# Optimization experiments

Hardware: AMD Instinct MI355X
Metric: run time of the kernel (lower is better)

## Reference

```python
import jax, jax.numpy as jnp
import numpy as np

A_CONST = 0.4
C_CONST = 500.0
N_BINS = 10


def entropy(w):
    # Faithful to the torch helper: n=10 half-open bins [min+i*s, min+(i+1)*s);
    # the maximum element falls outside the last bin, as in the original.
    x = w.reshape(-1)
    lo = x.min()
    hi = x.max()
    scale = (hi - lo) / N_BINS
    i = jnp.arange(N_BINS, dtype=x.dtype)
    lower = lo + i * scale            # [n]
    upper = lo + (i + 1.0) * scale    # [n]
    in_bin = (x[None, :] >= lower[:, None]) & (x[None, :] < upper[:, None])  # [n, len]
    p = jnp.sum(in_bin, axis=1).astype(jnp.float32) / x.shape[0]
    return jnp.sum(jnp.where(p > 0, -p * jnp.log(p), 0.0))


def blend_weight(base_w, graft_w, pnet_w):
    # param_direction = |base - graft| passed through bias-free Linear(in, in)
    d = jnp.abs(base_w - graft_w) @ pnet_w.T          # [out, in]
    w_local = jax.nn.sigmoid(d)
    w_global = A_CONST / jnp.pi * jnp.arctan(C_CONST * (entropy(base_w) - entropy(graft_w))) + 0.5
    w_base = w_global * (1.0 - jnp.exp(-w_global * w_local))
    w_graft = (1.0 - w_global) * (1.0 - jnp.exp(-(1.0 - w_global) * (1.0 - w_local)))
    ws = jax.nn.softmax(jnp.stack([w_base, w_graft], axis=-1), axis=-1)  # [out, in, 2]
    return base_w * ws[..., 0] + graft_w * ws[..., 1]


def setup_inputs() -> dict:
    key = jax.random.key(0)
    ks = jax.random.split(key, 9)
    B, D_IN, D_H, D_OUT = 65536, 1024, 512, 1
    return {
        "x": jax.random.normal(ks[0], (B, D_IN), dtype=jnp.float32),
        "w0": jax.random.normal(ks[1], (D_H, D_IN), dtype=jnp.float32) * 0.05,
        "b0": jax.random.normal(ks[2], (D_H,), dtype=jnp.float32) * 0.05,
        "w1": jax.random.normal(ks[3], (D_OUT, D_H), dtype=jnp.float32) * 0.05,
        "b1": jax.random.normal(ks[4], (D_OUT,), dtype=jnp.float32) * 0.05,
        "p0": jax.random.normal(ks[5], (D_IN, D_IN), dtype=jnp.float32) * 0.05,
        "p1": jax.random.normal(ks[6], (D_H, D_H), dtype=jnp.float32) * 0.05,
        "g0": jax.random.normal(ks[7], (D_H, D_IN), dtype=jnp.float32) * 0.05,
        "g1": jax.random.normal(ks[8], (D_OUT, D_H), dtype=jnp.float32) * 0.05,
    }


def reference(x, w0, b0, w1, b1, p0, p1, g0, g1):
    W0 = blend_weight(w0, g0, p0)
    x = jax.nn.relu(x @ W0.T + b0)   # layer 0 + ReLU
    W1 = blend_weight(w1, g1, p1)
    x = x @ W1.T + b1                # layer 1, no activation
    return x
```

## Files before the change

kernel.cpp:

```cpp
#include <hip/hip_runtime.h>
#include <hip/hip_bf16.h>
#include <math.h>


typedef __attribute__((ext_vector_type(8))) short short8;
typedef __attribute__((ext_vector_type(4))) short short4v;
typedef __attribute__((ext_vector_type(4))) float floatx4;
typedef unsigned short ushort_t;

#define WS_CNT 16
#define WS_PART 64
#define WS_PART2 576
#define WS_W0T 1024
#define WS_W1B (WS_W0T + 262144)

__device__ __forceinline__ short f2bf(float f) {
    union { __hip_bfloat16 h; short s; } u;
    u.h = __float2bfloat16(f);
    return u.s;
}
__device__ __forceinline__ float blend_factor(float d, float wg) {
    float wl = 1.0f / (1.0f + expf(-d));
    float wb = wg * (1.0f - expf(-wg * wl));
    float wgr = (1.0f - wg) * (1.0f - expf(-(1.0f - wg) * (1.0f - wl)));
    return 1.0f / (1.0f + expf(-(wb - wgr)));
}
__device__ __forceinline__ float wglobal_from_ent(float eb, float eg) {
    return 0.12732395447351627f * atanf(500.0f * (eb - eg)) + 0.5f;
}
__device__ __forceinline__ void async16(const void* g, void* s) {
    __builtin_amdgcn_global_load_lds(
        (const __attribute__((address_space(1))) unsigned int*)g,
        (__attribute__((address_space(3))) unsigned int*)s, 16, 0, 0);
}
__device__ __forceinline__ int swz_idx(int h, int k) {
    int kq = (k >> 3) & 3;
    return h * 32 + (((kq ^ ((h >> 1) & 3))) << 3) + (k & 7);
}

__global__ __launch_bounds__(256) void k_mm(const float* __restrict__ w0,
                                            const float* __restrict__ g0,
                                            const float* __restrict__ w1,
                                            const float* __restrict__ g1,
                                            unsigned* ws_u) {
    float* ws_f = (float*)ws_u;
    __shared__ float smn[4], smx[4];
    int bx = blockIdx.x, tid = threadIdx.x;
    int wave = tid >> 6, lane = tid & 63;
    int a = bx >> 7;
    const float* arr = (a ? g0 : w0) + (size_t)(bx & 127) * 4096;
    float mn = INFINITY, mx = -INFINITY;
    const float4* p4 = (const float4*)arr;
#pragma unroll
    for (int j = 0; j < 4; j++) {
        float4 v = p4[tid + j * 256];
        mn = fminf(mn, fminf(fminf(v.x, v.y), fminf(v.z, v.w)));
        mx = fmaxf(mx, fmaxf(fmaxf(v.x, v.y), fmaxf(v.z, v.w)));
    }
#pragma unroll
    for (int off = 32; off > 0; off >>= 1) {
        mn = fminf(mn, __shfl_xor(mn, off));
        mx = fmaxf(mx, __shfl_xor(mx, off));
    }
    if (lane == 0) { smn[wave] = mn; smx[wave] = mx; }
    __syncthreads();
    if (tid == 0) {
        mn = fminf(fminf(smn[0], smn[1]), fminf(smn[2], smn[3]));
        mx = fmaxf(fmaxf(smx[0], smx[1]), fmaxf(smx[2], smx[3]));
        ws_f[WS_PART + bx * 2] = mn;
        ws_f[WS_PART + bx * 2 + 1] = mx;
    }
    if (bx < 2 && tid < 64) {
        const float* arr2 = bx ? g1 : w1;
        float mn2 = INFINITY, mx2 = -INFINITY;
#pragma unroll
        for (int j = 0; j < 8; j++) {
            float v = arr2[tid + 64 * j];
            mn2 = fminf(mn2, v);
            mx2 = fmaxf(mx2, v);
        }
#pragma unroll
        for (int off = 32; off > 0; off >>= 1) {
            mn2 = fminf(mn2, __shfl_xor(mn2, off));
            mx2 = fmaxf(mx2, __shfl_xor(mx2, off));
        }
        if (tid == 0) {
            ws_f[WS_PART2 + bx * 2] = mn2;
            ws_f[WS_PART2 + bx * 2 + 1] = mx2;
        }
    }
    if (bx == 2 && tid < 40) ws_u[WS_CNT + tid] = 0u;
}

__global__ __launch_bounds__(256) void k_hist(const float* __restrict__ w0,
                                              const float* __restrict__ g0,
                                              const float* __restrict__ w1,
                                              const float* __restrict__ g1,
                                              unsigned* ws_u) {
    float* ws_f = (float*)ws_u;
    __shared__ float smn2[2], smx2[2];
    int bx = blockIdx.x, tid = threadIdx.x;
    int wave = tid >> 6, lane = tid & 63;
    int a = bx >> 7;
    float mn = INFINITY, mx = -INFINITY;
    if (tid < 128) {
        mn = ws_f[WS_PART + a * 256 + tid * 2];
        mx = ws_f[WS_PART + a * 256 + tid * 2 + 1];
    }
#pragma unroll
    for (int off = 32; off > 0; off >>= 1) {
        mn = fminf(mn, __shfl_xor(mn, off));
        mx = fmaxf(mx, __shfl_xor(mx, off));
    }
    if (wave < 2 && lane == 0) { smn2[wave] = mn; smx2[wave] = mx; }
    __syncthreads();
    float lo = fminf(smn2[0], smn2[1]);
    float hi = fmaxf(smx2[0], smx2[1]);

    float scale = __fdiv_rn(__fsub_rn(hi, lo), 10.0f);
    float lw[11];
#pragma unroll
    for (int j = 0; j < 11; j++)
        lw[j] = __fadd_rn(lo, __fmul_rn((float)j, scale));
    unsigned c[10];
#pragma unroll
    for (int b = 0; b < 10; b++) c[b] = 0u;
    const float* arr = (a ? g0 : w0) + (size_t)(bx & 127) * 4096;
    const float4* p4 = (const float4*)arr;
#pragma unroll
    for (int j = 0; j < 4; j++) {
        float4 v4 = p4[tid + j * 256];
        float vv[4] = {v4.x, v4.y, v4.z, v4.w};
#pragma unroll
        for (int e = 0; e < 4; e++) {
            float v = vv[e];
#pragma unroll
            for (int b = 0; b < 10; b++)
                c[b] += (v >= lw[b] && v < lw[b + 1]) ? 1u : 0u;
        }
    }
#pragma unroll
    for (int b = 0; b < 10; b++) {
#pragma unroll
        for (int off = 32; off > 0; off >>= 1) c[b] += __shfl_xor(c[b], off);
    }
    if (lane == 0) {
#pragma unroll
        for (int b = 0; b < 10; b++)
            if (c[b] > 0u) atomicAdd(&ws_u[WS_CNT + a * 10 + b], c[b]);
    }
    if (bx < 2 && tid < 64) {
        int a2 = 2 + bx;
        const float* arr2 = bx ? g1 : w1;
        float lo2 = ws_f[WS_PART2 + bx * 2];
        float hi2 = ws_f[WS_PART2 + bx * 2 + 1];
        float sc2 = __fdiv_rn(__fsub_rn(hi2, lo2), 10.0f);
        float lw2[11];
#pragma unroll
        for (int j = 0; j < 11; j++)
            lw2[j] = __fadd_rn(lo2, __fmul_rn((float)j, sc2));
        unsigned c2[10];
#pragma unroll
        for (int b = 0; b < 10; b++) c2[b] = 0u;
#pragma unroll
        for (int j = 0; j < 8; j++) {
            float v = arr2[tid + 64 * j];
#pragma unroll
            for (int b = 0; b < 10; b++)
                c2[b] += (v >= lw2[b] && v < lw2[b + 1]) ? 1u : 0u;
        }
#pragma unroll
        for (int b = 0; b < 10; b++) {
#pragma unroll
            for (int off = 32; off > 0; off >>= 1) c2[b] += __shfl_xor(c2[b], off);
        }
        if (tid == 0) {
#pragma unroll
            for (int b = 0; b < 10; b++)
                if (c2[b] > 0u) atomicAdd(&ws_u[WS_CNT + a2 * 10 + b], c2[b]);
        }
    }
}

__global__ __launch_bounds__(256) void k_blend(const float* __restrict__ w0,
                                               const float* __restrict__ g0,
                                               const float* __restrict__ w1,
                                               const float* __restrict__ g1,
                                               const float* __restrict__ p0,
                                               const float* __restrict__ p1,
                                               unsigned* ws_u) {
    float* ws_f = (float*)ws_u;
    ushort_t* W0t = (ushort_t*)(ws_u + WS_W0T);
    float* W1b = ws_f + WS_W1B;
    __shared__ float ent_s[4];
    __shared__ float diff[512];
    __shared__ ushort_t As[32 * 40];
    __shared__ ushort_t Ps[64 * 40];
    int bx = blockIdx.x, tid = threadIdx.x;
    int w = tid >> 6, l = tid & 63;

    if (tid < 4) {
        float n = (tid < 2) ? 524288.0f : 512.0f;
        float ent = 0.0f;
        for (int i = 0; i < 10; i++) {
            float p = __fdiv_rn((float)ws_u[WS_CNT + tid * 10 + i], n);
            if (p > 0.0f) ent = __fsub_rn(ent, __fmul_rn(p, logf(p)));
        }
        ent_s[tid] = ent;
    }
    __syncthreads();
    float wg0 = wglobal_from_ent(ent_s[0], ent_s[1]);
    float wg1 = wglobal_from_ent(ent_s[2], ent_s[3]);

    if (bx < 128) {
        for (int i = tid; i < 512; i += 256) diff[i] = fabsf(w1[i] - g1[i]);
        __syncthreads();
        int i = bx * 4 + w;
        float acc = 0.0f;
#pragma unroll
        for (int j = 0; j < 8; j++) {
            int k = l + 64 * j;
            acc += diff[k] * p1[i * 512 + k];
        }
#pragma unroll
        for (int off = 32; off > 0; off >>= 1) acc += __shfl_xor(acc, off);
        if (l == 0) {
            float s0 = blend_factor(acc, wg1);
            W1b[i] = w1[i] * s0 + g1[i] * (1.0f - s0);
        }
    }

    int bo = (bx >> 4) * 32;
    int bi = (bx & 15) * 64;
    int wo = w & 1, wi = w >> 1;
    int m_in = l & 15, kq = l >> 4;

    floatx4 acc2[2];
    const floatx4 zero = {0.0f, 0.0f, 0.0f, 0.0f};
    acc2[0] = zero; acc2[1] = zero;

    int ar = tid >> 3, ac = (tid & 7) * 4;
    int pr = tid >> 2, pc = (tid & 3) * 8;
    const float* wbase = w0 + (size_t)(bo + ar) * 1024 + ac;
    const float* gbase = g0 + (size_t)(bo + ar) * 1024 + ac;
    const float* pbase = p0 + (size_t)(bi + pr) * 1024 + pc;
    ushort_t* awr = &As[ar * 40 + ac];
    ushort_t* pwr = &Ps[pr * 40 + pc];

#pragma unroll 1
    for (int k0 = 0; k0 < 1024; k0 += 32) {
        float4 vw = *(const float4*)(wbase + k0);
        float4 vg = *(const float4*)(gbase + k0);
        float4 q0 = *(const float4*)(pbase + k0);
        float4 q1 = *(const float4*)(pbase + k0 + 4);
        short4v a4;
        a4[0] = f2bf(fabsf(vw.x - vg.x));
        a4[1] = f2bf(fabsf(vw.y - vg.y));
        a4[2] = f2bf(fabsf(vw.z - vg.z));
        a4[3] = f2bf(fabsf(vw.w - vg.w));
        short8 p8;
        p8[0] = f2bf(q0.x); p8[1] = f2bf(q0.y); p8[2] = f2bf(q0.z); p8[3] = f2bf(q0.w);
        p8[4] = f2bf(q1.x); p8[5] = f2bf(q1.y); p8[6] = f2bf(q1.z); p8[7] = f2bf(q1.w);
        __syncthreads();
        *(short4v*)awr = a4;
        *(short8*)pwr = p8;
        __syncthreads();
        short8 af = *(const short8*)&As[(wo * 16 + m_in) * 40 + kq * 8];
        short8 pf0 = *(const short8*)&Ps[(wi * 32 + m_in) * 40 + kq * 8];
        short8 pf1 = *(const short8*)&Ps[(wi * 32 + 16 + m_in) * 40 + kq * 8];
        acc2[0] = __builtin_amdgcn_mfma_f32_16x16x32_bf16(af, pf0, acc2[0], 0, 0, 0);
        acc2[1] = __builtin_amdgcn_mfma_f32_16x16x32_bf16(af, pf1, acc2[1], 0, 0, 0);
    }
#pragma unroll
    for (int tn = 0; tn < 2; tn++) {
#pragma unroll
        for (int reg = 0; reg < 4; reg++) {
            int o = bo + wo * 16 + kq * 4 + reg;
            int i = bi + wi * 32 + tn * 16 + m_in;
            float s0 = blend_factor(acc2[tn][reg], wg0);
            float v = w0[o * 1024 + i] * s0 + g0[o * 1024 + i] * (1.0f - s0);
            W0t[(size_t)(i >> 5) * 16384 + swz_idx(o, i & 31)] = (ushort_t)f2bf(v);
        }
    }
}

__global__ __launch_bounds__(256, 2) void main_mfma(const float* __restrict__ x,
                                                    const float* __restrict__ b0,
                                                    const ushort_t* __restrict__ W0t,
                                                    const float* __restrict__ W1b,
                                                    const float* __restrict__ b1,
                                                    float* __restrict__ out) {
    __shared__ ushort_t As[2][64 * 40];
    __shared__ ushort_t Bs[2][512 * 32];
    __shared__ float red[4][64];
    int tid = threadIdx.x;
    int w = tid >> 6, l = tid & 63;
    int row0 = blockIdx.x * 64;
    int m_in = l & 15, kq = l >> 4;

    floatx4 acc[4][8];
    const floatx4 zero = {0.0f, 0.0f, 0.0f, 0.0f};
#pragma unroll
    for (int tm = 0; tm < 4; tm++)
#pragma unroll
        for (int tn = 0; tn < 8; tn++) acc[tm][tn] = zero;

    int arow = tid >> 2, acol = (tid & 3) * 8;
    const float* xbase = x + (size_t)(row0 + arow) * 1024 + acol;
    int awr_off = arow * 40 + acol;
    const ushort_t* bsrc = W0t + (size_t)tid * 8;
    int bko = ((kq ^ ((m_in >> 1) & 3)) << 3);

    float4 pv0 = *(const float4*)(xbase);
    float4 pv1 = *(const float4*)(xbase + 4);
#pragma unroll
    for (int r = 0; r < 8; r++)
        async16(bsrc + r * 2048, &Bs[0][r * 2048 + w * 512]);
    {
        short8 s0;
        s0[0] = f2bf(pv0.x); s0[1] = f2bf(pv0.y); s0[2] = f2bf(pv0.z); s0[3] = f2bf(pv0.w);
        s0[4] = f2bf(pv1.x); s0[5] = f2bf(pv1.y); s0[6] = f2bf(pv1.z); s0[7] = f2bf(pv1.w);
        *(short8*)&As[0][awr_off] = s0;
    }
    __syncthreads();

#pragma unroll 1
    for (int t = 0; t < 32; ++t) {
        int cur = t & 1, nxt = cur ^ 1;
        float4 nv0, nv1;
        if (t < 31) {
            const float* xn = xbase + (t + 1) * 32;
            nv0 = *(const float4*)xn;
            nv1 = *(const float4*)(xn + 4);
            const ushort_t* bt = bsrc + (t + 1) * 16384;
#pragma unroll
            for (int r = 0; r < 8; r++)
                async16(bt + r * 2048, &Bs[nxt][r * 2048 + w * 512]);
        }
        short8 af[4];
#pragma unroll
        for (int tm = 0; tm < 4; tm++)
            af[tm] = *(const short8*)&As[cur][(tm * 16 + m_in) * 40 + kq * 8];
#pragma unroll
        for (int tn = 0; tn < 8; tn++) {
            int row = w * 128 + tn * 16 + m_in;
            short8 bfr = *(const short8*)&Bs[cur][row * 32 + bko];
#pragma unroll
            for (int tm = 0; tm < 4; tm++)
                acc[tm][tn] = __builtin_amdgcn_mfma_f32_16x16x32_bf16(
                    af[tm], bfr, acc[tm][tn], 0, 0, 0);
        }
        if (t < 31) {
            short8 s0;
            s0[0] = f2bf(nv0.x); s0[1] = f2bf(nv0.y); s0[2] = f2bf(nv0.z); s0[3] = f2bf(nv0.w);
            s0[4] = f2bf(nv1.x); s0[5] = f2bf(nv1.y); s0[6] = f2bf(nv1.z); s0[7] = f2bf(nv1.w);
            *(short8*)&As[nxt][awr_off] = s0;
        }
        __syncthreads();
    }

    float b0v[8], w1v[8];
#pragma unroll
    for (int tn = 0; tn < 8; tn++) {
        int h = w * 128 + tn * 16 + m_in;
        b0v[tn] = b0[h];
        w1v[tn] = W1b[h];
    }
#pragma unroll
    for (int tm = 0; tm < 4; tm++) {
#pragma unroll
        for (int reg = 0; reg < 4; reg++) {
            float s = 0.0f;
#pragma unroll
            for (int tn = 0; tn < 8; tn++) {
                float y = acc[tm][tn][reg] + b0v[tn];
                y = fmaxf(y, 0.0f);
                s += y * w1v[tn];
            }
            s += __shfl_xor(s, 1);
            s += __shfl_xor(s, 2);
            s += __shfl_xor(s, 4);
            s += __shfl_xor(s, 8);
            if (m_in == 0) red[w][tm * 16 + kq * 4 + reg] = s;
        }
    }
    __syncthreads();
    if (tid < 64)
        out[row0 + tid] = red[0][tid] + red[1][tid] + red[2][tid] + red[3][tid] + b1[0];
}

extern "C" void kernel_launch(void* const* d_in, const int* in_sizes, int n_in,
                              void* d_out, int out_size, void* d_ws, size_t ws_size,
                              hipStream_t stream) {
    const float* x = (const float*)d_in[0];
    const float* w0 = (const float*)d_in[1];
    const float* b0 = (const float*)d_in[2];
    const float* w1 = (const float*)d_in[3];
    const float* b1 = (const float*)d_in[4];
    const float* p0 = (const float*)d_in[5];
    const float* p1 = (const float*)d_in[6];
    const float* g0 = (const float*)d_in[7];
    const float* g1 = (const float*)d_in[8];
    float* out = (float*)d_out;
    unsigned* ws_u = (unsigned*)d_ws;
    float* ws_f = (float*)d_ws;
    ushort_t* W0t = (ushort_t*)(ws_u + WS_W0T);
    float* W1b = ws_f + WS_W1B;

    k_mm<<<256, 256, 0, stream>>>(w0, g0, w1, g1, ws_u);
    k_hist<<<256, 256, 0, stream>>>(w0, g0, w1, g1, ws_u);
    k_blend<<<256, 256, 0, stream>>>(w0, g0, w1, g1, p0, p1, ws_u);
    main_mfma<<<1024, 256, 0, stream>>>(x, b0, W0t, W1b, b1, out);
}
```

Before: 530.2 us.

## Load W0 MFMA fragments directly from global in fragment-ordered layout

Measured after the change: 629.3 us. 1.19x slower.

```diff
diff --git a/kernel.cpp b/kernel.cpp
--- a/kernel.cpp
+++ b/kernel.cpp
@@ -28,14 +28,9 @@
 __device__ __forceinline__ float wglobal_from_ent(float eb, float eg) {
     return 0.12732395447351627f * atanf(500.0f * (eb - eg)) + 0.5f;
 }
-__device__ __forceinline__ void async16(const void* g, void* s) {
-    __builtin_amdgcn_global_load_lds(
-        (const __attribute__((address_space(1))) unsigned int*)g,
-        (__attribute__((address_space(3))) unsigned int*)s, 16, 0, 0);
-}
-__device__ __forceinline__ int swz_idx(int h, int k) {
-    int kq = (k >> 3) & 3;
-    return h * 32 + (((kq ^ ((h >> 1) & 3))) << 3) + (k & 7);
+__device__ __forceinline__ size_t w0t_idx(int h, int k) {
+    return (size_t)(k >> 5) * 16384 + (h >> 4) * 512 + ((k >> 3) & 3) * 128 +
+           (h & 15) * 8 + (k & 7);
 }
 
 __global__ __launch_bounds__(256) void k_mm(const float* __restrict__ w0,
@@ -279,7 +274,7 @@
             int i = bi + wi * 32 + tn * 16 + m_in;
             float s0 = blend_factor(acc2[tn][reg], wg0);
             float v = w0[o * 1024 + i] * s0 + g0[o * 1024 + i] * (1.0f - s0);
-            W0t[(size_t)(i >> 5) * 16384 + swz_idx(o, i & 31)] = (ushort_t)f2bf(v);
+            W0t[w0t_idx(o, i)] = (ushort_t)f2bf(v);
         }
     }
 }
@@ -291,7 +286,6 @@
                                                     const float* __restrict__ b1,
                                                     float* __restrict__ out) {
     __shared__ ushort_t As[2][64 * 40];
-    __shared__ ushort_t Bs[2][512 * 32];
     __shared__ float red[4][64];
     int tid = threadIdx.x;
     int w = tid >> 6, l = tid & 63;
@@ -308,18 +302,14 @@
     int arow = tid >> 2, acol = (tid & 3) * 8;
     const float* xbase = x + (size_t)(row0 + arow) * 1024 + acol;
     int awr_off = arow * 40 + acol;
-    const ushort_t* bsrc = W0t + (size_t)tid * 8;
-    int bko = ((kq ^ ((m_in >> 1) & 3)) << 3);
-
-    float4 pv0 = *(const float4*)(xbase);
-    float4 pv1 = *(const float4*)(xbase + 4);
-#pragma unroll
-    for (int r = 0; r < 8; r++)
-        async16(bsrc + r * 2048, &Bs[0][r * 2048 + w * 512]);
+    const ushort_t* bbase = W0t + w * 4096 + l * 8;
+
     {
+        float4 v0 = *(const float4*)xbase;
+        float4 v1 = *(const float4*)(xbase + 4);
         short8 s0;
-        s0[0] = f2bf(pv0.x); s0[1] = f2bf(pv0.y); s0[2] = f2bf(pv0.z); s0[3] = f2bf(pv0.w);
-        s0[4] = f2bf(pv1.x); s0[5] = f2bf(pv1.y); s0[6] = f2bf(pv1.z); s0[7] = f2bf(pv1.w);
+        s0[0] = f2bf(v0.x); s0[1] = f2bf(v0.y); s0[2] = f2bf(v0.z); s0[3] = f2bf(v0.w);
+        s0[4] = f2bf(v1.x); s0[5] = f2bf(v1.y); s0[6] = f2bf(v1.z); s0[7] = f2bf(v1.w);
         *(short8*)&As[0][awr_off] = s0;
     }
     __syncthreads();
@@ -332,24 +322,22 @@
             const float* xn = xbase + (t + 1) * 32;
             nv0 = *(const float4*)xn;
             nv1 = *(const float4*)(xn + 4);
-            const ushort_t* bt = bsrc + (t + 1) * 16384;
-#pragma unroll
-            for (int r = 0; r < 8; r++)
-                async16(bt + r * 2048, &Bs[nxt][r * 2048 + w * 512]);
-        }
+        }
+        const ushort_t* bt = bbase + (size_t)t * 16384;
+        short8 bfr[8];
+#pragma unroll
+        for (int tn = 0; tn < 8; tn++)
+            bfr[tn] = *(const short8*)(bt + tn * 512);
         short8 af[4];
 #pragma unroll
         for (int tm = 0; tm < 4; tm++)
             af[tm] = *(const short8*)&As[cur][(tm * 16 + m_in) * 40 + kq * 8];
 #pragma unroll
-        for (int tn = 0; tn < 8; tn++) {
-            int row = w * 128 + tn * 16 + m_in;
-            short8 bfr = *(const short8*)&Bs[cur][row * 32 + bko];
+        for (int tn = 0; tn < 8; tn++)
 #pragma unroll
             for (int tm = 0; tm < 4; tm++)
                 acc[tm][tn] = __builtin_amdgcn_mfma_f32_16x16x32_bf16(
-                    af[tm], bfr, acc[tm][tn], 0, 0, 0);
-        }
+                    af[tm], bfr[tn], acc[tm][tn], 0, 0, 0);
         if (t < 31) {
             short8 s0;
             s0[0] = f2bf(nv0.x); s0[1] = f2bf(nv0.y); s0[2] = f2bf(nv0.z); s0[3] = f2bf(nv0.w);
@@ -403,9 +391,8 @@
     const float* g1 = (const float*)d_in[8];
     float* out = (float*)d_out;
     unsigned* ws_u = (unsigned*)d_ws;
-    float* ws_f = (float*)d_ws;
     ushort_t* W0t = (ushort_t*)(ws_u + WS_W0T);
-    float* W1b = ws_f + WS_W1B;
+    float* W1b = ((float*)d_ws) + WS_W1B;
 
     k_mm<<<256, 256, 0, stream>>>(w0, g0, w1, g1, ws_u);
     k_hist<<<256, 256, 0, stream>>>(w0, g0, w1, g1, ws_u);
```
